# Optimization experiments

Measured on AMD Instinct MI355X. Metric: run time of the kernel, lower is better.

## Reference

```python
import jax, jax.numpy as jnp
import numpy as np

B, N, K, D, H, L = 2, 2048, 256, 768, 150, 11
REL_PROP = 2
NB = 10  # distance buckets


def _lin(key, din, dout):
    return jax.random.normal(key, (din, dout), dtype=jnp.float32) / np.sqrt(din)


def setup_inputs() -> dict:
    key = jax.random.key(0)
    ks = jax.random.split(key, 16)
    rng = np.random.default_rng(0)
    prune_idx = jnp.asarray(np.stack([np.sort(rng.permutation(N)[:K]) for _ in range(B)]), dtype=jnp.int32)
    span_begin = jnp.sort(jax.random.randint(ks[2], (B, K), 0, N - 16), axis=-1).astype(jnp.int32)
    span_end = (span_begin + jax.random.randint(ks[3], (B, K), 1, 16)).astype(jnp.int32)
    return {
        "all_span_vecs": jax.random.normal(ks[0], (B, N, D), dtype=jnp.float32),
        "update": jax.random.normal(ks[1], (B, K, D), dtype=jnp.float32),
        "square_mask": jnp.ones((B, K, K), dtype=jnp.float32),
        "span_lengths": jnp.full((B,), float(K), dtype=jnp.float32),
        "span_begin": span_begin,
        "span_end": span_end,
        "prune_indices": prune_idx,
        "w_left": _lin(ks[4], D, H), "b_left": jnp.zeros((H,), jnp.float32),
        "w_right": _lin(ks[5], D, H), "b_right": jnp.zeros((H,), jnp.float32),
        "dist_emb": jax.random.normal(ks[6], (NB, H), dtype=jnp.float32) * 0.02,
        "w_h": _lin(ks[7], H, H), "b_h": jnp.zeros((H,), jnp.float32),
        "w_out": _lin(ks[8], H, L), "b_out": jnp.zeros((L,), jnp.float32),
        "a_w": _lin(ks[9], L, D),
        "gate_w": _lin(ks[10], 2 * D, D), "gate_b": jnp.zeros((D,), jnp.float32),
        "pr_w": _lin(ks[11], D, 1), "pr_b": jnp.zeros((1,), jnp.float32),
    }


def _pair_scores(u, bins, w_left, b_left, w_right, b_right, dist_emb, w_h, b_h, w_out, b_out):
    # OptFFpairs: left/right span projections + pairwise distance embedding -> FF -> L labels
    left = u @ w_left + b_left          # [B,K,H]
    right = u @ w_right + b_right       # [B,K,H]
    h = jax.nn.relu(left[:, :, None, :] + right[:, None, :, :] + dist_emb[bins])  # [B,K,K,H]
    h = jax.nn.relu(h @ w_h + b_h)
    return h @ w_out + b_out            # [B,K,K,L]


def _add_unary(rel, ss):
    # relation_add_scores: add per-span pruner scores along both pair axes; ss: [B,K,1]
    return rel + ss[:, :, None, :] + ss[:, None, :, :]


def reference(all_span_vecs, update, square_mask, span_lengths, span_begin, span_end,
              prune_indices, w_left, b_left, w_right, b_right, dist_emb, w_h, b_h,
              w_out, b_out, a_w, gate_w, gate_b, pr_w, pr_b):
    bins = jnp.clip(jnp.abs(span_begin[:, None, :] - span_begin[:, :, None]), 0, NB - 1)  # [B,K,K]
    rel = _pair_scores(update, bins, w_left, b_left, w_right, b_right, dist_emb, w_h, b_h, w_out, b_out)
    rel = _add_unary(rel, update @ pr_w + pr_b)
    for _ in range(REL_PROP):
        probs = jax.nn.relu(rel) * square_mask[..., None]     # [B,K,K,L]
        msg = probs @ a_w                                     # A(probs): [B,K,K,D]
        # ctxt[b,j,d] = sum_i msg[b,i,j,d] * update[b,i,d] / span_lengths[b]
        ctxt = (msg * update[:, :, None, :]).sum(-3) / span_lengths[:, None, None]
        g = jax.nn.sigmoid(jnp.concatenate([update, ctxt], axis=-1) @ gate_w + gate_b)
        update = g * update + (1.0 - g) * ctxt                # MyGate
        rel = _pair_scores(update, bins, w_left, b_left, w_right, b_right, dist_emb, w_h, b_h, w_out, b_out)
        rel = _add_unary(rel, update @ pr_w + pr_b)           # pruner.scorer(update)
    # overwrite_spans: scatter updated filtered spans back into the full span tensor
    valid = jnp.arange(K)[None, :] < span_lengths[:, None]    # [B,K]
    bidx = jnp.arange(B)[:, None]
    orig = all_span_vecs[bidx, prune_indices]                 # [B,K,D]
    vals = jnp.where(valid[..., None], update, orig)
    update_all = all_span_vecs.at[bidx, prune_indices].set(vals)
    return update_all, update, rel
```

## Files before the change

### kernel.cpp

```cpp
#include <hip/hip_runtime.h>
#include <hip/hip_bf16.h>
#include <math.h>

#define BB 2
#define NN 2048
#define KK 256
#define DD 768
#define HH 150
#define LL 11
#define NBINS 10

#define KP 160
#define WP 40
#define GWP 72
#define BPAD 264

typedef __attribute__((ext_vector_type(8))) short short8;
typedef __attribute__((ext_vector_type(4))) short s16x4;
typedef __attribute__((ext_vector_type(4))) float f32x4;

__device__ inline unsigned bf2u(float lo, float hi) {
  union { __hip_bfloat162 b; unsigned u; } cv;
  cv.b = __float22bfloat162_rn(make_float2(lo, hi));
  return cv.u;
}
__device__ inline short bf1(float x) {
  union { __hip_bfloat16 b; short s; } cv;
  cv.b = __float2bfloat16(x);
  return cv.s;
}

#define PRE_PREP 110
#define PRE_CVT  1536
#define PRE_TRGW 1152
#define PRE_TRWLR 240
#define PRE_TRUPD 384
#define PRE_NB (PRE_PREP + PRE_CVT + PRE_TRGW + PRE_TRWLR + PRE_TRUPD)

__global__ __launch_bounds__(256) void k_pre(
    const float* __restrict__ w_h, const float* __restrict__ w_out,
    short* __restrict__ wt, short* __restrict__ wo,
    const float* __restrict__ upd_in, short* __restrict__ updbf,
    const float* __restrict__ gate_w, short* __restrict__ gwt,
    const float* __restrict__ w_left, const float* __restrict__ w_right,
    short* __restrict__ wlrt, short* __restrict__ updT)
{
  __shared__ float tile[32][33];
  int bid = blockIdx.x;
  int t = threadIdx.x;

  if (bid < PRE_PREP) {
    int idx = bid * 256 + t;
    if (idx < KP * KP) {
      int n = idx / KP, k = idx - n * KP;
      float v = (n < HH && k < HH) ? w_h[k * HH + n] : 0.f;
      wt[idx] = bf1(v);
    }
    int idx2 = idx - KP * KP;
    if (idx2 >= 0 && idx2 < 16 * KP) {
      int n = idx2 / KP, k = idx2 - n * KP;
      float v = (n < LL && k < HH) ? w_out[k * LL + n] : 0.f;
      wo[idx2] = bf1(v);
    }
    return;
  }
  bid -= PRE_PREP;
  if (bid < PRE_CVT) {
    int idx = bid * 256 + t;
    if (idx < BB * KK * DD) updbf[idx] = bf1(upd_in[idx]);
    return;
  }
  bid -= PRE_CVT;
  if (bid < PRE_TRGW) {
    int kt = bid % 48, nt = bid / 48;
    int m0 = kt * 32, n0 = nt * 32;
    int tx = t & 31, ty = t >> 5;
    #pragma unroll
    for (int r = 0; r < 4; ++r)
      tile[ty + r * 8][tx] = gate_w[(size_t)(m0 + ty + r * 8) * DD + n0 + tx];
    __syncthreads();
    #pragma unroll
    for (int r = 0; r < 4; ++r)
      gwt[(size_t)(n0 + ty + r * 8) * (2 * DD) + m0 + tx] = bf1(tile[tx][ty + r * 8]);
    return;
  }
  bid -= PRE_TRGW;
  if (bid < PRE_TRWLR) {
    int kt = bid % 24, nt = bid / 24;
    int k0 = kt * 32, n0 = nt * 32;
    const float* src = (n0 >= KP) ? w_right : w_left;
    int col0 = n0 - (n0 >= KP ? KP : 0);
    int tx = t & 31, ty = t >> 5;
    #pragma unroll
    for (int r = 0; r < 4; ++r) {
      int col = col0 + tx;
      tile[ty + r * 8][tx] = (col < HH) ? src[(size_t)(k0 + ty + r * 8) * HH + col] : 0.f;
    }
    __syncthreads();
    #pragma unroll
    for (int r = 0; r < 4; ++r)
      wlrt[(size_t)(n0 + ty + r * 8) * DD + k0 + tx] = bf1(tile[tx][ty + r * 8]);
    return;
  }
  bid -= PRE_TRWLR;
  {
    int b = bid / 192;
    int r = bid - b * 192;
    int it = r & 7, dt = r >> 3;
    int i0 = it * 32, d0 = dt * 32;
    int tx = t & 31, ty = t >> 5;
    #pragma unroll
    for (int rr = 0; rr < 4; ++rr)
      tile[ty + rr * 8][tx] = upd_in[(size_t)(b * KK + i0 + ty + rr * 8) * DD + d0 + tx];
    __syncthreads();
    #pragma unroll
    for (int rr = 0; rr < 4; ++rr)
      updT[(size_t)(b * DD + d0 + ty + rr * 8) * KK + i0 + tx] = bf1(tile[tx][ty + rr * 8]);
  }
}

__global__ __launch_bounds__(256) void k_projss(
    const short* __restrict__ updbf, const short* __restrict__ wlrt,
    const float* __restrict__ b_left, const float* __restrict__ b_right,
    const float* __restrict__ updf, const float* __restrict__ pr_w,
    const float* __restrict__ pr_b,
    float* __restrict__ left, float* __restrict__ right, float* __restrict__ ssv)
{
  __shared__ short As[64][WP];
  __shared__ short Bs[KP][WP];
  int bidx = blockIdx.x;
  int t = threadIdx.x;

  if (bidx >= 16) {
    int row = (bidx - 16) * 4 + (t >> 6);
    int l = t & 63;
    float s = 0.f;
    for (int d = l; d < DD; d += 64) s = fmaf(updf[(size_t)row * DD + d], pr_w[d], s);
    #pragma unroll
    for (int off = 32; off > 0; off >>= 1) s += __shfl_down(s, off);
    if (l == 0) ssv[row] = s + pr_b[0];
    return;
  }

  int rbk = bidx >> 1, half = bidx & 1;
  int row0 = rbk * 64;
  const short* wsrc = wlrt + (size_t)half * KP * DD;
  int l = t & 63, w = t >> 6, lr = l & 15, lg = l >> 4;
  int ar = t >> 2, ac = t & 3;
  int i1 = t + 256, i2 = t + 512;
  f32x4 acc[10];
  #pragma unroll
  for (int nt = 0; nt < 10; ++nt) acc[nt] = (f32x4){0.f, 0.f, 0.f, 0.f};

  short8 pa, pb0, pb1, pb2 = {};
  pa  = *(const short8*)(updbf + (size_t)(row0 + ar) * DD + ac * 8);
  pb0 = *(const short8*)(wsrc + (size_t)(t >> 2) * DD + (t & 3) * 8);
  pb1 = *(const short8*)(wsrc + (size_t)(i1 >> 2) * DD + (i1 & 3) * 8);
  if (i2 < 640) pb2 = *(const short8*)(wsrc + (size_t)(i2 >> 2) * DD + (i2 & 3) * 8);

  for (int ks = 0; ks < 24; ++ks) {
    __syncthreads();
    *(short8*)&As[ar][ac * 8] = pa;
    *(short8*)&Bs[t >> 2][(t & 3) * 8] = pb0;
    *(short8*)&Bs[i1 >> 2][(i1 & 3) * 8] = pb1;
    if (i2 < 640) *(short8*)&Bs[i2 >> 2][(i2 & 3) * 8] = pb2;
    __syncthreads();
    if (ks + 1 < 24) {
      int k0 = (ks + 1) * 32;
      pa  = *(const short8*)(updbf + (size_t)(row0 + ar) * DD + k0 + ac * 8);
      pb0 = *(const short8*)(wsrc + (size_t)(t >> 2) * DD + k0 + (t & 3) * 8);
      pb1 = *(const short8*)(wsrc + (size_t)(i1 >> 2) * DD + k0 + (i1 & 3) * 8);
      if (i2 < 640) pb2 = *(const short8*)(wsrc + (size_t)(i2 >> 2) * DD + k0 + (i2 & 3) * 8);
    }
    short8 a = *(short8*)&As[w * 16 + lr][lg * 8];
    #pragma unroll
    for (int nt = 0; nt < 10; ++nt) {
      short8 b = *(short8*)&Bs[nt * 16 + lr][lg * 8];
      acc[nt] = __builtin_amdgcn_mfma_f32_16x16x32_bf16(a, b, acc[nt], 0, 0, 0);
    }
  }
  const float* bias = half ? b_right : b_left;
  float* dst = half ? right : left;
  int rowb = row0 + w * 16 + lg * 4;
  #pragma unroll
  for (int nt = 0; nt < 10; ++nt) {
    int col = nt * 16 + lr;
    if (col < HH) {
      float bv = bias[col];
      #pragma unroll
      for (int q = 0; q < 4; ++q)
        dst[(size_t)(rowb + q) * HH + col] = acc[nt][q] + bv;
    }
  }
}

template <bool WPT>
__global__ __launch_bounds__(256, 4) void k_pair_mfma(
    const float* __restrict__ left, const float* __restrict__ right,
    const float* __restrict__ ss, const int* __restrict__ span_begin,
    const float* __restrict__ demb,
    const short* __restrict__ wt, const short* __restrict__ wo,
    const float* __restrict__ b_h, const float* __restrict__ b_out,
    const float* __restrict__ mask,
    float* __restrict__ rel, short* __restrict__ probsT)
{
  int bid = blockIdx.x;
  int b  = bid >> 10;
  int r2 = bid & 1023;
  int i  = r2 >> 2;
  int j0 = (r2 & 3) * 64;

  __shared__ short wtbuf[2][32 * KP];
  __shared__ float ld_s[NBINS][KP];
  __shared__ float bh_s[KP];
  __shared__ float ssj_s[64];
  __shared__ float m_s[64];
  __shared__ int   bins[64];

  int t = threadIdx.x;
  int l = t & 63, w = t >> 6;
  int lr = l & 15, lg = l >> 4;

  int sbi = span_begin[b * KK + i];
  if (t < 64) {
    int d = span_begin[b * KK + j0 + t] - sbi; d = d < 0 ? -d : d;
    bins[t] = d > NBINS - 1 ? NBINS - 1 : d;
    ssj_s[t] = ss[b * KK + j0 + t];
    if (WPT) m_s[t] = mask[((size_t)(b * KK + i)) * KK + j0 + t];
  }
  for (int idx = t; idx < KP; idx += 256) bh_s[idx] = (idx < HH) ? b_h[idx] : 0.f;
  {
    const float* lrow = left + (size_t)(b * KK + i) * HH;
    for (int idx = t; idx < NBINS * KP; idx += 256) {
      int bn = idx / KP, k = idx - bn * KP;
      ld_s[bn][k] = (k < HH) ? (lrow[k] + demb[bn * HH + k]) : 0.f;
    }
  }
  short8 wo_f[5];
  #pragma unroll
  for (int ks = 0; ks < 5; ++ks)
    wo_f[ks] = *(const short8*)(wo + lr * KP + ks * 32 + lg * 8);

  short8 pw[3];
  #pragma unroll
  for (int c = 0; c < 3; ++c) {
    int idx = t + c * 256;
    if (idx < 640) pw[c] = *(const short8*)(wt + idx * 8);
  }
  #pragma unroll
  for (int c = 0; c < 3; ++c) {
    int idx = t + c * 256;
    if (idx < 640) *(short8*)&wtbuf[0][idx * 8] = pw[c];
  }
  #pragma unroll
  for (int c = 0; c < 3; ++c) {
    int idx = t + c * 256;
    if (idx < 640) pw[c] = *(const short8*)(wt + 5120 + idx * 8);
  }
  __syncthreads();

  int jr = w * 16 + lr;
  int binr = bins[jr];
  const float* rrow = right + (size_t)(b * KK + j0 + jr) * HH;
  const float* ldr = &ld_s[binr][0];
  short8 afr[5];
  #pragma unroll
  for (int ks = 0; ks < 5; ++ks) {
    unsigned pk[4];
    #pragma unroll
    for (int e = 0; e < 4; ++e) {
      int k = ks * 32 + lg * 8 + e * 2;
      float2 r2v = (k < HH - 1) ? *(const float2*)(rrow + k) : make_float2(0.f, 0.f);
      float2 lv = *(const float2*)(ldr + k);
      float v0 = fmaxf(lv.x + r2v.x, 0.f);
      float v1 = fmaxf(lv.y + r2v.y, 0.f);
      pk[e] = bf2u(v0, v1);
    }
    int4 tmp; tmp.x = (int)pk[0]; tmp.y = (int)pk[1]; tmp.z = (int)pk[2]; tmp.w = (int)pk[3];
    afr[ks] = *(short8*)&tmp;
  }

  f32x4 acc[10];
  #pragma unroll
  for (int m = 0; m < 10; ++m) acc[m] = (f32x4){0.f, 0.f, 0.f, 0.f};

  #pragma unroll
  for (int s = 0; s < 5; ++s) {
    if (s > 0) __syncthreads();
    if (s + 1 < 5) {
      #pragma unroll
      for (int c = 0; c < 3; ++c) {
        int idx = t + c * 256;
        if (idx < 640) *(short8*)&wtbuf[(s + 1) & 1][idx * 8] = pw[c];
      }
      if (s + 2 < 5) {
        #pragma unroll
        for (int c = 0; c < 3; ++c) {
          int idx = t + c * 256;
          if (idx < 640) pw[c] = *(const short8*)(wt + (s + 2) * 5120 + idx * 8);
        }
      }
    }
    const short* bufp = &wtbuf[s & 1][0];
    #pragma unroll
    for (int ks = 0; ks < 5; ++ks) {
      short8 a = afr[ks];
      #pragma unroll
      for (int ntp = 0; ntp < 2; ++ntp) {
        short8 bf = *(const short8*)(bufp + (ntp * 16 + lr) * KP + ks * 32 + lg * 8);
        acc[s * 2 + ntp] = __builtin_amdgcn_mfma_f32_16x16x32_bf16(a, bf, acc[s * 2 + ntp], 0, 0, 0);
      }
    }
  }
  __syncthreads();

  short* h1 = &wtbuf[0][0];
  #pragma unroll
  for (int m = 0; m < 10; ++m) {
    int col = (m >> 1) * 32 + (m & 1) * 16 + lr;
    float bh = bh_s[col];
    #pragma unroll
    for (int q = 0; q < 4; ++q) {
      int row = w * 16 + lg * 4 + q;
      h1[row * KP + col] = bf1(fmaxf(acc[m][q] + bh, 0.f));
    }
  }
  __syncthreads();

  f32x4 acc2 = (f32x4){0.f, 0.f, 0.f, 0.f};
  #pragma unroll
  for (int ks = 0; ks < 5; ++ks) {
    short8 a = *(const short8*)(h1 + (w * 16 + lr) * KP + ks * 32 + lg * 8);
    acc2 = __builtin_amdgcn_mfma_f32_16x16x32_bf16(a, wo_f[ks], acc2, 0, 0, 0);
  }

  float ssi = ss[b * KK + i];
  float* out_s = (float*)&ld_s[0][0];
  if (lr < LL) {
    float bo = b_out[lr];
    #pragma unroll
    for (int q = 0; q < 4; ++q) {
      int row = w * 16 + lg * 4 + q;
      out_s[row * 12 + lr] = acc2[q] + bo + ssi + ssj_s[row];
    }
  }
  __syncthreads();
  size_t base = ((size_t)(b * KK + i) * KK + j0) * LL;
  for (int idx = t; idx < 64 * LL; idx += 256) {
    int j = idx / LL, ll2 = idx - j * LL;
    rel[base + idx] = out_s[j * 12 + ll2];
  }
  if (WPT) {
    for (int idx = t; idx < 64 * LL; idx += 256) {
      int j = idx / LL, ll2 = idx - j * LL;
      float v = fmaxf(out_s[j * 12 + ll2], 0.f) * m_s[j];
      probsT[(((size_t)(b * LL + ll2)) * KK + j0 + j) * KK + i] = bf1(v);
    }
  }
}

__global__ __launch_bounds__(256) void k_ctxt_mfma(
    const short* __restrict__ probsT, const short* __restrict__ updT,
    const float* __restrict__ a_w, const float* __restrict__ span_len,
    float* __restrict__ ctxt, short* __restrict__ ctxbf)
{
  int bidx = blockIdx.x;
  int b = bidx / 96;
  int r = bidx - b * 96;
  int jt = r / 12, dt = r - jt * 12;
  int j0 = jt * 32, d0 = dt * 64;

  __shared__ short Bs[64][BPAD];
  __shared__ short As[32][BPAD];

  int t = threadIdx.x, l = t & 63, w = t >> 6, lr = l & 15, lg = l >> 4;
  int wr = w >> 1, wc = w & 1;

  for (int s = 0; s < 8; ++s) {
    int idx = t + s * 256;
    int row = idx >> 5, c = idx & 31;
    *(short8*)&Bs[row][c * 8] =
        *(const short8*)(updT + ((size_t)(b * DD + d0 + row)) * KK + c * 8);
  }

  short8 pa[4];
  #pragma unroll
  for (int s = 0; s < 4; ++s) {
    int idx = t + s * 256;
    int row = idx >> 5, c = idx & 31;
    pa[s] = *(const short8*)(probsT + (((size_t)(b * LL + 0)) * KK + j0 + row) * KK + c * 8);
  }

  f32x4 accF[2];
  accF[0] = (f32x4){0.f, 0.f, 0.f, 0.f};
  accF[1] = (f32x4){0.f, 0.f, 0.f, 0.f};

  for (int ll = 0; ll < LL; ++ll) {
    __syncthreads();
    #pragma unroll
    for (int s = 0; s < 4; ++s) {
      int idx = t + s * 256;
      int row = idx >> 5, c = idx & 31;
      *(short8*)&As[row][c * 8] = pa[s];
    }
    if (ll + 1 < LL) {
      #pragma unroll
      for (int s = 0; s < 4; ++s) {
        int idx = t + s * 256;
        int row = idx >> 5, c = idx & 31;
        pa[s] = *(const short8*)(probsT + (((size_t)(b * LL + ll + 1)) * KK + j0 + row) * KK + c * 8);
      }
    }
    float awl[2];
    #pragma unroll
    for (int nt = 0; nt < 2; ++nt) awl[nt] = a_w[ll * DD + d0 + wc * 32 + nt * 16 + lr];
    __syncthreads();

    f32x4 accL[2];
    accL[0] = (f32x4){0.f, 0.f, 0.f, 0.f};
    accL[1] = (f32x4){0.f, 0.f, 0.f, 0.f};
    #pragma unroll
    for (int ks = 0; ks < 8; ++ks) {
      short8 a = *(short8*)&As[wr * 16 + lr][ks * 32 + lg * 8];
      #pragma unroll
      for (int nt = 0; nt < 2; ++nt) {
        short8 bf = *(short8*)&Bs[wc * 32 + nt * 16 + lr][ks * 32 + lg * 8];
        accL[nt] = __builtin_amdgcn_mfma_f32_16x16x32_bf16(a, bf, accL[nt], 0, 0, 0);
      }
    }
    #pragma unroll
    for (int nt = 0; nt < 2; ++nt)
      #pragma unroll
      for (int q = 0; q < 4; ++q)
        accF[nt][q] = fmaf(awl[nt], accL[nt][q], accF[nt][q]);
  }

  float inv = 1.f / span_len[b];
  int rowb = j0 + wr * 16 + lg * 4;
  #pragma unroll
  for (int nt = 0; nt < 2; ++nt) {
    int col = d0 + wc * 32 + nt * 16 + lr;
    #pragma unroll
    for (int q = 0; q < 4; ++q) {
      size_t off = (size_t)(b * KK + rowb + q) * DD + col;
      float v = accF[nt][q] * inv;
      ctxt[off] = v;
      ctxbf[off] = bf1(v);
    }
  }
}

__global__ __launch_bounds__(256) void k_gate_mfma(
    const short* __restrict__ updbf, const short* __restrict__ ctxbf,
    const short* __restrict__ gwt, const float* __restrict__ gate_b,
    const float* __restrict__ ctxt, float* __restrict__ upd,
    short* __restrict__ nxtbf, short* __restrict__ updT)
{
  int rb = blockIdx.x / 12, cb = blockIdx.x - rb * 12;
  int row0 = rb * 32, col0 = cb * 64;
  __shared__ short As[32][GWP];
  __shared__ short Bs[64][GWP];
  int t = threadIdx.x, l = t & 63, w = t >> 6, lr = l & 15, lg = l >> 4;
  int wr = w >> 1, wc = w & 1;

  int ar = t >> 3, ac = t & 7;
  int b1 = t + 256;

  f32x4 acc[2];
  acc[0] = (f32x4){0.f, 0.f, 0.f, 0.f};
  acc[1] = (f32x4){0.f, 0.f, 0.f, 0.f};

  short8 pa = *(const short8*)(updbf + (size_t)(row0 + ar) * DD + ac * 8);
  short8 pb0 = *(const short8*)(gwt + (size_t)(col0 + (t >> 3)) * (2 * DD) + (t & 7) * 8);
  short8 pb1 = *(const short8*)(gwt + (size_t)(col0 + (b1 >> 3)) * (2 * DD) + (b1 & 7) * 8);

  for (int ks = 0; ks < 24; ++ks) {
    __syncthreads();
    *(short8*)&As[ar][ac * 8] = pa;
    *(short8*)&Bs[t >> 3][(t & 7) * 8] = pb0;
    *(short8*)&Bs[b1 >> 3][(b1 & 7) * 8] = pb1;
    if (ks + 1 < 24) {
      int k0 = (ks + 1) * 64;
      int ka = k0 + ac * 8;
      const short* asrc = (ka < DD) ? (updbf + (size_t)(row0 + ar) * DD + ka)
                                    : (ctxbf + (size_t)(row0 + ar) * DD + ka - DD);
      pa  = *(const short8*)asrc;
      pb0 = *(const short8*)(gwt + (size_t)(col0 + (t >> 3)) * (2 * DD) + k0 + (t & 7) * 8);
      pb1 = *(const short8*)(gwt + (size_t)(col0 + (b1 >> 3)) * (2 * DD) + k0 + (b1 & 7) * 8);
    }
    __syncthreads();
    #pragma unroll
    for (int ksub = 0; ksub < 2; ++ksub) {
      short8 a = *(short8*)&As[wr * 16 + lr][ksub * 32 + lg * 8];
      #pragma unroll
      for (int nt = 0; nt < 2; ++nt) {
        short8 bf = *(short8*)&Bs[wc * 32 + nt * 16 + lr][ksub * 32 + lg * 8];
        acc[nt] = __builtin_amdgcn_mfma_f32_16x16x32_bf16(a, bf, acc[nt], 0, 0, 0);
      }
    }
  }
  int rowb = row0 + wr * 16 + lg * 4;
  int bb = rowb >> 8, ii = rowb & 255;
  #pragma unroll
  for (int nt = 0; nt < 2; ++nt) {
    int col = col0 + wc * 32 + nt * 16 + lr;
    float gb = gate_b[col];
    s16x4 tw;
    #pragma unroll
    for (int q = 0; q < 4; ++q) {
      size_t off = (size_t)(rowb + q) * DD + col;
      float x = acc[nt][q] + gb;
      float g = 1.f / (1.f + expf(-x));
      float o = g * upd[off] + (1.f - g) * ctxt[off];
      upd[off] = o;
      short bv = bf1(o);
      nxtbf[off] = bv;
      tw[q] = bv;
    }
    *(s16x4*)(updT + ((size_t)(bb * DD + col)) * KK + ii) = tw;
  }
}

__global__ void k_scatter(const float* __restrict__ upd,
                          const int* __restrict__ prune_idx,
                          const float* __restrict__ span_len,
                          float* __restrict__ out_all)
{
  int b = blockIdx.x / KK;
  int k = blockIdx.x - b * KK;
  if ((float)k < span_len[b]) {
    int dst = prune_idx[b * KK + k];
    const float4* src = (const float4*)(upd + ((size_t)(b * KK + k)) * DD);
    float4* d = (float4*)(out_all + ((size_t)b * NN + dst) * DD);
    for (int idx = threadIdx.x; idx < DD / 4; idx += blockDim.x) d[idx] = src[idx];
  }
}

extern "C" void kernel_launch(void* const* d_in, const int* in_sizes, int n_in,
                              void* d_out, int out_size, void* d_ws, size_t ws_size,
                              hipStream_t stream)
{
  (void)in_sizes; (void)n_in; (void)out_size; (void)ws_size;
  const float* all_span = (const float*)d_in[0];
  const float* upd_in   = (const float*)d_in[1];
  const float* mask     = (const float*)d_in[2];
  const float* span_len = (const float*)d_in[3];
  const int*   span_beg = (const int*)d_in[4];
  const int*   prune    = (const int*)d_in[6];
  const float* w_left   = (const float*)d_in[7];
  const float* b_left   = (const float*)d_in[8];
  const float* w_right  = (const float*)d_in[9];
  const float* b_right  = (const float*)d_in[10];
  const float* dist_emb = (const float*)d_in[11];
  const float* w_h      = (const float*)d_in[12];
  const float* b_h      = (const float*)d_in[13];
  const float* w_out    = (const float*)d_in[14];
  const float* b_out    = (const float*)d_in[15];
  const float* a_w      = (const float*)d_in[16];
  const float* gate_w   = (const float*)d_in[17];
  const float* gate_b   = (const float*)d_in[18];
  const float* pr_w     = (const float*)d_in[19];
  const float* pr_b     = (const float*)d_in[20];

  float* out_all = (float*)d_out;
  float* out_upd = out_all + (size_t)BB * NN * DD;
  float* out_rel = out_upd + (size_t)BB * KK * DD;

  float* ws     = (float*)d_ws;
  float* left   = ws;
  float* right  = left + (size_t)BB * KK * HH;
  float* ssv    = right + (size_t)BB * KK * HH + 64;
  float* ctxt   = ssv + (size_t)BB * KK;
  short* wt_bf  = (short*)(ctxt + (size_t)BB * KK * DD);
  short* wo_bf  = wt_bf + KP * KP;
  short* updbf0 = wo_bf + 16 * KP;
  short* updbf1 = updbf0 + (size_t)BB * KK * DD;
  short* ctxbf  = updbf1 + (size_t)BB * KK * DD;
  short* gwt    = ctxbf + (size_t)BB * KK * DD;
  short* wlrt   = gwt + (size_t)DD * 2 * DD;
  short* probsT = wlrt + (size_t)2 * KP * DD;
  short* updT   = probsT + (size_t)BB * LL * KK * KK;

  hipMemcpyAsync(out_all, all_span, sizeof(float) * (size_t)BB * NN * DD,
                 hipMemcpyDeviceToDevice, stream);
  hipMemcpyAsync(out_upd, upd_in, sizeof(float) * (size_t)BB * KK * DD,
                 hipMemcpyDeviceToDevice, stream);
  k_pre<<<PRE_NB, 256, 0, stream>>>(w_h, w_out, wt_bf, wo_bf, upd_in, updbf0,
                                    gate_w, gwt, w_left, w_right, wlrt, updT);

  k_projss<<<144, 256, 0, stream>>>(updbf0, wlrt, b_left, b_right, out_upd,
                                    pr_w, pr_b, left, right, ssv);
  k_pair_mfma<true><<<BB * KK * 4, 256, 0, stream>>>(
      left, right, ssv, span_beg, dist_emb, wt_bf, wo_bf, b_h, b_out, mask,
      out_rel, probsT);

  for (int p = 0; p < 2; ++p) {
    short* cur_bf = (p == 0) ? updbf0 : updbf1;
    short* nxt_bf = (p == 0) ? updbf1 : updbf0;
    k_ctxt_mfma<<<BB * 8 * 12, 256, 0, stream>>>(probsT, updT, a_w, span_len, ctxt, ctxbf);
    k_gate_mfma<<<16 * 12, 256, 0, stream>>>(cur_bf, ctxbf, gwt, gate_b, ctxt,
                                             out_upd, nxt_bf, updT);
    k_projss<<<144, 256, 0, stream>>>(nxt_bf, wlrt, b_left, b_right, out_upd,
                                      pr_w, pr_b, left, right, ssv);
    if (p == 0) {
      k_pair_mfma<true><<<BB * KK * 4, 256, 0, stream>>>(
          left, right, ssv, span_beg, dist_emb, wt_bf, wo_bf, b_h, b_out, mask,
          out_rel, probsT);
    } else {
      k_pair_mfma<false><<<BB * KK * 4, 256, 0, stream>>>(
          left, right, ssv, span_beg, dist_emb, wt_bf, wo_bf, b_h, b_out, mask,
          out_rel, probsT);
    }
  }
  k_scatter<<<BB * KK, 192, 0, stream>>>(out_upd, prune, span_len, out_all);
}
```

Baseline: 194.8 us.

## Drop fp32 ctxt buffer and update copy; widen gate GEMM K-step to 128

The context kernel now writes only the bf16 context, and the gate kernel reads the context back from bf16 instead of a separate fp32 buffer, removing one fp32 write and read per propagation step. The device-to-device copy of the input update into the output is removed: the first gate pass reads the original input and writes the output buffer directly, and the first projection reads the input too. The gate GEMM stages 128-wide K tiles, which halves the number of barrier-separated iterations at the cost of more LDS and registers. Reading the context from bf16 lowers the precision of the gating blend.

```diff
diff --git a/kernel.cpp b/kernel.cpp
--- a/kernel.cpp
+++ b/kernel.cpp
@@ -12,7 +12,7 @@
 
 #define KP 160
 #define WP 40
-#define GWP 72
+#define GWP 136
 #define BPAD 264
 
 typedef __attribute__((ext_vector_type(8))) short short8;
@@ -28,6 +28,9 @@
   union { __hip_bfloat16 b; short s; } cv;
   cv.b = __float2bfloat16(x);
   return cv.s;
+}
+__device__ inline float ubf(short b) {
+  return __uint_as_float(((unsigned)(unsigned short)b) << 16);
 }
 
 #define PRE_PREP 110
@@ -362,7 +365,7 @@
 __global__ __launch_bounds__(256) void k_ctxt_mfma(
     const short* __restrict__ probsT, const short* __restrict__ updT,
     const float* __restrict__ a_w, const float* __restrict__ span_len,
-    float* __restrict__ ctxt, short* __restrict__ ctxbf)
+    short* __restrict__ ctxbf)
 {
   int bidx = blockIdx.x;
   int b = bidx / 96;
@@ -443,9 +446,7 @@
     #pragma unroll
     for (int q = 0; q < 4; ++q) {
       size_t off = (size_t)(b * KK + rowb + q) * DD + col;
-      float v = accF[nt][q] * inv;
-      ctxt[off] = v;
-      ctxbf[off] = bf1(v);
+      ctxbf[off] = bf1(accF[nt][q] * inv);
     }
   }
 }
@@ -453,7 +454,7 @@
 __global__ __launch_bounds__(256) void k_gate_mfma(
     const short* __restrict__ updbf, const short* __restrict__ ctxbf,
     const short* __restrict__ gwt, const float* __restrict__ gate_b,
-    const float* __restrict__ ctxt, float* __restrict__ upd,
+    const float* __restrict__ updr, float* __restrict__ updw,
     short* __restrict__ nxtbf, short* __restrict__ updT)
 {
   int rb = blockIdx.x / 12, cb = blockIdx.x - rb * 12;
@@ -463,34 +464,53 @@
   int t = threadIdx.x, l = t & 63, w = t >> 6, lr = l & 15, lg = l >> 4;
   int wr = w >> 1, wc = w & 1;
 
-  int ar = t >> 3, ac = t & 7;
-  int b1 = t + 256;
-
   f32x4 acc[2];
   acc[0] = (f32x4){0.f, 0.f, 0.f, 0.f};
   acc[1] = (f32x4){0.f, 0.f, 0.f, 0.f};
 
-  short8 pa = *(const short8*)(updbf + (size_t)(row0 + ar) * DD + ac * 8);
-  short8 pb0 = *(const short8*)(gwt + (size_t)(col0 + (t >> 3)) * (2 * DD) + (t & 7) * 8);
-  short8 pb1 = *(const short8*)(gwt + (size_t)(col0 + (b1 >> 3)) * (2 * DD) + (b1 & 7) * 8);
-
-  for (int ks = 0; ks < 24; ++ks) {
-    __syncthreads();
-    *(short8*)&As[ar][ac * 8] = pa;
-    *(short8*)&Bs[t >> 3][(t & 7) * 8] = pb0;
-    *(short8*)&Bs[b1 >> 3][(b1 & 7) * 8] = pb1;
-    if (ks + 1 < 24) {
-      int k0 = (ks + 1) * 64;
-      int ka = k0 + ac * 8;
-      const short* asrc = (ka < DD) ? (updbf + (size_t)(row0 + ar) * DD + ka)
-                                    : (ctxbf + (size_t)(row0 + ar) * DD + ka - DD);
-      pa  = *(const short8*)asrc;
-      pb0 = *(const short8*)(gwt + (size_t)(col0 + (t >> 3)) * (2 * DD) + k0 + (t & 7) * 8);
-      pb1 = *(const short8*)(gwt + (size_t)(col0 + (b1 >> 3)) * (2 * DD) + k0 + (b1 & 7) * 8);
-    }
-    __syncthreads();
-    #pragma unroll
-    for (int ksub = 0; ksub < 2; ++ksub) {
+  short8 pa[2], pb[4];
+  #pragma unroll
+  for (int s = 0; s < 2; ++s) {
+    int idx = t + s * 256;
+    pa[s] = *(const short8*)(updbf + (size_t)(row0 + (idx >> 4)) * DD + (idx & 15) * 8);
+  }
+  #pragma unroll
+  for (int s = 0; s < 4; ++s) {
+    int idx = t + s * 256;
+    pb[s] = *(const short8*)(gwt + (size_t)(col0 + (idx >> 4)) * (2 * DD) + (idx & 15) * 8);
+  }
+
+  for (int ph = 0; ph < 12; ++ph) {
+    __syncthreads();
+    #pragma unroll
+    for (int s = 0; s < 2; ++s) {
+      int idx = t + s * 256;
+      *(short8*)&As[idx >> 4][(idx & 15) * 8] = pa[s];
+    }
+    #pragma unroll
+    for (int s = 0; s < 4; ++s) {
+      int idx = t + s * 256;
+      *(short8*)&Bs[idx >> 4][(idx & 15) * 8] = pb[s];
+    }
+    if (ph + 1 < 12) {
+      int k0 = (ph + 1) * 128;
+      #pragma unroll
+      for (int s = 0; s < 2; ++s) {
+        int idx = t + s * 256;
+        int ka = k0 + (idx & 15) * 8;
+        const short* asrc = (ka < DD) ? (updbf + (size_t)(row0 + (idx >> 4)) * DD + ka)
+                                      : (ctxbf + (size_t)(row0 + (idx >> 4)) * DD + ka - DD);
+        pa[s] = *(const short8*)asrc;
+      }
+      #pragma unroll
+      for (int s = 0; s < 4; ++s) {
+        int idx = t + s * 256;
+        pb[s] = *(const short8*)(gwt + (size_t)(col0 + (idx >> 4)) * (2 * DD) + k0 + (idx & 15) * 8);
+      }
+    }
+    __syncthreads();
+    #pragma unroll
+    for (int ksub = 0; ksub < 4; ++ksub) {
       short8 a = *(short8*)&As[wr * 16 + lr][ksub * 32 + lg * 8];
       #pragma unroll
       for (int nt = 0; nt < 2; ++nt) {
@@ -511,8 +531,9 @@
       size_t off = (size_t)(rowb + q) * DD + col;
       float x = acc[nt][q] + gb;
       float g = 1.f / (1.f + expf(-x));
-      float o = g * upd[off] + (1.f - g) * ctxt[off];
-      upd[off] = o;
+      float cv = ubf(ctxbf[off]);
+      float o = g * updr[off] + (1.f - g) * cv;
+      updw[off] = o;
       short bv = bf1(o);
       nxtbf[off] = bv;
       tw[q] = bv;
@@ -570,8 +591,7 @@
   float* left   = ws;
   float* right  = left + (size_t)BB * KK * HH;
   float* ssv    = right + (size_t)BB * KK * HH + 64;
-  float* ctxt   = ssv + (size_t)BB * KK;
-  short* wt_bf  = (short*)(ctxt + (size_t)BB * KK * DD);
+  short* wt_bf  = (short*)(ssv + (size_t)BB * KK);
   short* wo_bf  = wt_bf + KP * KP;
   short* updbf0 = wo_bf + 16 * KP;
   short* updbf1 = updbf0 + (size_t)BB * KK * DD;
@@ -583,12 +603,10 @@
 
   hipMemcpyAsync(out_all, all_span, sizeof(float) * (size_t)BB * NN * DD,
                  hipMemcpyDeviceToDevice, stream);
-  hipMemcpyAsync(out_upd, upd_in, sizeof(float) * (size_t)BB * KK * DD,
-                 hipMemcpyDeviceToDevice, stream);
   k_pre<<<PRE_NB, 256, 0, stream>>>(w_h, w_out, wt_bf, wo_bf, upd_in, updbf0,
                                     gate_w, gwt, w_left, w_right, wlrt, updT);
 
-  k_projss<<<144, 256, 0, stream>>>(updbf0, wlrt, b_left, b_right, out_upd,
+  k_projss<<<144, 256, 0, stream>>>(updbf0, wlrt, b_left, b_right, upd_in,
                                     pr_w, pr_b, left, right, ssv);
   k_pair_mfma<true><<<BB * KK * 4, 256, 0, stream>>>(
       left, right, ssv, span_beg, dist_emb, wt_bf, wo_bf, b_h, b_out, mask,
@@ -597,9 +615,10 @@
   for (int p = 0; p < 2; ++p) {
     short* cur_bf = (p == 0) ? updbf0 : updbf1;
     short* nxt_bf = (p == 0) ? updbf1 : updbf0;
-    k_ctxt_mfma<<<BB * 8 * 12, 256, 0, stream>>>(probsT, updT, a_w, span_len, ctxt, ctxbf);
-    k_gate_mfma<<<16 * 12, 256, 0, stream>>>(cur_bf, ctxbf, gwt, gate_b, ctxt,
-                                             out_upd, nxt_bf, updT);
+    const float* updr = (p == 0) ? upd_in : out_upd;
+    k_ctxt_mfma<<<BB * 8 * 12, 256, 0, stream>>>(probsT, updT, a_w, span_len, ctxbf);
+    k_gate_mfma<<<16 * 12, 256, 0, stream>>>(cur_bf, ctxbf, gwt, gate_b,
+                                             updr, out_upd, nxt_bf, updT);
     k_projss<<<144, 256, 0, stream>>>(nxt_bf, wlrt, b_left, b_right, out_upd,
                                       pr_w, pr_b, left, right, ssv);
     if (p == 0) {
```

Result: no change. 191.5 us (-1.7%).
